# Kernel tuning notes

Measured on AMD Instinct MI355X. Metric: run time of the kernel, lower is better.

Reference implementation:

```python
import jax, jax.numpy as jnp
import numpy as np

N_NODES = 100000


def gcn_conv(x, edge_index, W, b):
    """PyG GCNConv: h = x W^T; add self-loops; symmetric deg^-1/2 norm; scatter-add; + bias."""
    n = x.shape[0]
    src = jnp.concatenate([edge_index[0], jnp.arange(n)])  # self-loops appended
    dst = jnp.concatenate([edge_index[1], jnp.arange(n)])
    deg = jax.ops.segment_sum(jnp.ones_like(dst, dtype=x.dtype), dst, num_segments=n)
    dinv = jnp.where(deg > 0, jax.lax.rsqrt(deg), 0.0)
    norm = dinv[src] * dinv[dst]                             # [E+n]
    h = x @ W.T                                              # [n, out]
    msg = norm[:, None] * h[src]                             # [E+n, out] gather
    out = jax.ops.segment_sum(msg, dst, num_segments=n)      # scatter-add
    return out + b


def setup_inputs() -> dict:
    key = jax.random.key(0)
    ks = jax.random.split(key, 10)
    input_dim, gnn_hidden, tree_hidden, num_classes = 128, 64, 32, 8
    n_edges = 3200000
    x = jax.random.normal(ks[0], (N_NODES, input_dim), dtype=jnp.float32)
    edge_index = jax.random.randint(ks[1], (2, n_edges), 0, N_NODES, dtype=jnp.int64)
    # GCNConv params (PyG Linear weight is [out, in], glorot-ish scale)
    W1 = jax.random.normal(ks[2], (gnn_hidden, input_dim), dtype=jnp.float32) / np.sqrt(input_dim)
    b1 = jnp.zeros((gnn_hidden,), dtype=jnp.float32)
    W2 = jax.random.normal(ks[3], (tree_hidden, gnn_hidden), dtype=jnp.float32) / np.sqrt(gnn_hidden)
    b2 = jnp.zeros((tree_hidden,), dtype=jnp.float32)
    # SoftDecisionTree params (torch.randn init in source)
    gate_w = jax.random.normal(ks[4], (tree_hidden, tree_hidden), dtype=jnp.float32)
    gate_b = jnp.zeros((tree_hidden,), dtype=jnp.float32)
    leaf_w = jax.random.normal(ks[5], (tree_hidden, num_classes), dtype=jnp.float32)
    return {"x": x, "edge_index": edge_index, "W1": W1, "b1": b1, "W2": W2,
            "b2": b2, "gate_w": gate_w, "gate_b": gate_b, "leaf_w": leaf_w}


def reference(x, edge_index, W1, b1, W2, b2, gate_w, gate_b, leaf_w):
    h = jax.nn.relu(gcn_conv(x, edge_index, W1, b1))
    h = gcn_conv(h, edge_index, W2, b2)
    gates = jax.nn.sigmoid(h @ gate_w.T + gate_b)
    return gates @ leaf_w
```

## Files before the change

### kernel.cpp

```cpp
#include <hip/hip_runtime.h>
#include <math.h>

#define IN_DIM 128
#define H1 64
#define H2 32
#define NC 8
#define SCAN_CH 1024
#define NB_MAX 512

typedef unsigned int u32;

__device__ __forceinline__ float bf_lo(u32 u) { return __uint_as_float(u << 16); }
__device__ __forceinline__ float bf_hi(u32 u) { return __uint_as_float(u & 0xffff0000u); }
__device__ __forceinline__ unsigned short f2b(float f) {
  u32 u = __float_as_uint(f);
  u += 0x7fffu + ((u >> 16) & 1u);
  return (unsigned short)(u >> 16);
}


__global__ __launch_bounds__(256) void k_hist(const int* __restrict__ dst,
                                              int* __restrict__ bh,
                                              int E, int EPB, int NBk, int BLK) {
  __shared__ int h[NB_MAX];
  int k = blockIdx.x, tid = threadIdx.x;
  for (int i = tid; i < NBk; i += 256) h[i] = 0;
  __syncthreads();
  int st = k * EPB, en = min(E, st + EPB);
  for (int i = st + tid; i < en; i += 256)
    atomicAdd(&h[((u32)dst[i]) >> 8], 1);
  __syncthreads();
  for (int b = tid; b < NBk; b += 256) bh[b * BLK + k] = h[b];
}


__global__ __launch_bounds__(256) void k_gsc1(const int* __restrict__ A,
                                              int* __restrict__ bsum, int L) {
  int b = blockIdx.x, tid = threadIdx.x;
  int i0 = b * SCAN_CH + tid * 4;
  int s = 0;
  if (i0 + 3 < L) {
    int4 v = *(const int4*)(A + i0);
    s = v.x + v.y + v.z + v.w;
  } else {
    for (int i = i0; i < L; ++i) s += A[i];
  }
  __shared__ int red[256];
  red[tid] = s;
  __syncthreads();
  for (int d = 128; d > 0; d >>= 1) {
    if (tid < d) red[tid] += red[tid + d];
    __syncthreads();
  }
  if (tid == 0) bsum[b] = red[0];
}

__global__ __launch_bounds__(256) void k_gsc2(const int* __restrict__ bsum,
                                              int* __restrict__ bbase,
                                              int* __restrict__ S, int nbk, int L) {
  __shared__ int part[256];
  int tid = threadIdx.x;
  int chunk = (nbk + 255) / 256;
  int st = tid * chunk, en = min(st + chunk, nbk);
  int s = 0;
  for (int i = st; i < en; ++i) s += bsum[i];
  part[tid] = s;
  __syncthreads();
  for (int d = 1; d < 256; d <<= 1) {
    int t = (tid >= d) ? part[tid - d] : 0;
    __syncthreads();
    part[tid] += t;
    __syncthreads();
  }
  int base = (tid == 0) ? 0 : part[tid - 1];
  for (int i = st; i < en; ++i) { bbase[i] = base; base += bsum[i]; }
  if (tid == 255) S[L] = part[255];
}

__global__ __launch_bounds__(256) void k_gsc3(const int* __restrict__ A,
                                              const int* __restrict__ bbase,
                                              int* __restrict__ S, int L) {
  int b = blockIdx.x, tid = threadIdx.x;
  int i0 = b * SCAN_CH + tid * 4;
  int e0 = 0, e1 = 0, e2 = 0, e3 = 0;
  if (i0 + 3 < L) {
    int4 v = *(const int4*)(A + i0);
    e0 = v.x; e1 = v.y; e2 = v.z; e3 = v.w;
  } else {
    if (i0 + 0 < L) e0 = A[i0 + 0];
    if (i0 + 1 < L) e1 = A[i0 + 1];
    if (i0 + 2 < L) e2 = A[i0 + 2];
    if (i0 + 3 < L) e3 = A[i0 + 3];
  }
  __shared__ int part[256];
  part[tid] = e0 + e1 + e2 + e3;
  __syncthreads();
  for (int d = 1; d < 256; d <<= 1) {
    int t = (tid >= d) ? part[tid - d] : 0;
    __syncthreads();
    part[tid] += t;
    __syncthreads();
  }
  int base = bbase[b] + ((tid == 0) ? 0 : part[tid - 1]);
  int o0 = base, o1 = o0 + e0, o2 = o1 + e1, o3 = o2 + e2;
  if (i0 + 3 < L) {
    int4 o; o.x = o0; o.y = o1; o.z = o2; o.w = o3;
    *(int4*)(S + i0) = o;
  } else {
    if (i0 + 0 < L) S[i0 + 0] = o0;
    if (i0 + 1 < L) S[i0 + 1] = o1;
    if (i0 + 2 < L) S[i0 + 2] = o2;
    if (i0 + 3 < L) S[i0 + 3] = o3;
  }
}


__global__ __launch_bounds__(256) void k_scatter(const int* __restrict__ src,
                                                 const int* __restrict__ dst,
                                                 const int* __restrict__ S,
                                                 u32* __restrict__ packed,
                                                 int E, int EPB, int NBk, int BLK) {
  __shared__ int cur[NB_MAX];
  int k = blockIdx.x, tid = threadIdx.x;
  for (int b = tid; b < NBk; b += 256) cur[b] = S[b * BLK + k];
  __syncthreads();
  int st = k * EPB, en = min(E, st + EPB);
  for (int i = st + tid; i < en; i += 256) {
    int d = dst[i];
    int b = ((u32)d) >> 8;
    int pos = atomicAdd(&cur[b], 1);
    packed[pos] = (((u32)d & 255u) << 17) | (u32)src[i];
  }
}


__global__ __launch_bounds__(256) void k_build(const u32* __restrict__ packed,
                                               const int* __restrict__ S,
                                               int* __restrict__ csr,
                                               int* __restrict__ off,
                                               float* __restrict__ dinv,
                                               int n, int NBk, int BLK) {
  __shared__ int cnt[256];
  __shared__ int tmp[256];
  __shared__ int curh[256];
  int b = blockIdx.x, tid = threadIdx.x;
  int r0 = S[b * BLK];
  int r1 = S[(b + 1) * BLK];
  cnt[tid] = 0;
  __syncthreads();
  for (int i = r0 + tid; i < r1; i += 256)
    atomicAdd(&cnt[packed[i] >> 17], 1);
  __syncthreads();
  int v = cnt[tid];
  tmp[tid] = v;
  __syncthreads();
  for (int d = 1; d < 256; d <<= 1) {
    int t = (tid >= d) ? tmp[tid - d] : 0;
    __syncthreads();
    tmp[tid] += t;
    __syncthreads();
  }
  int base = r0 + tmp[tid] - v;
  int node = b * 256 + tid;
  if (node < n) {
    off[node] = base;
    dinv[node] = rsqrtf((float)(v + 1));
  }
  if (b == NBk - 1 && tid == 0) off[n] = r1;
  curh[tid] = base;
  __syncthreads();
  for (int i = r0 + tid; i < r1; i += 256) {
    u32 u = packed[i];
    int pos = atomicAdd(&curh[u >> 17], 1);
    csr[pos] = (int)(u & 0x1FFFFu);
  }
}


__global__ void k_proj1(const float4* __restrict__ x4, const float* __restrict__ W1,
                        const float* __restrict__ dinv,
                        unsigned short* __restrict__ h1p, int n) {
  __shared__ float xs[16][IN_DIM];
  __shared__ float wt[IN_DIM][H1 + 1];
  int tid = threadIdx.x;
  int row0 = blockIdx.x * 16;

  for (int i = tid; i < (H1 * IN_DIM / 4); i += 256) {
    float4 w = ((const float4*)W1)[i];
    int o = (i * 4) / IN_DIM;
    int k = (i * 4) % IN_DIM;
    wt[k + 0][o] = w.x; wt[k + 1][o] = w.y; wt[k + 2][o] = w.z; wt[k + 3][o] = w.w;
  }
  for (int i = tid; i < 16 * IN_DIM / 4; i += 256) {
    int r = (i * 4) / IN_DIM, k = (i * 4) % IN_DIM;
    int row = row0 + r;
    if (row < n)
      *((float4*)&xs[r][k]) = x4[(size_t)row * (IN_DIM / 4) + k / 4];
  }
  __syncthreads();

  int o = tid & 63, rq = tid >> 6;
  float a0 = 0.f, a1 = 0.f, a2 = 0.f, a3 = 0.f;
  for (int k = 0; k < IN_DIM; ++k) {
    float w = wt[k][o];
    a0 += xs[rq * 4 + 0][k] * w;
    a1 += xs[rq * 4 + 1][k] * w;
    a2 += xs[rq * 4 + 2][k] * w;
    a3 += xs[rq * 4 + 3][k] * w;
  }
  int r = row0 + rq * 4;
  if (r + 0 < n) h1p[(size_t)(r + 0) * H1 + o] = f2b(a0 * dinv[r + 0]);
  if (r + 1 < n) h1p[(size_t)(r + 1) * H1 + o] = f2b(a1 * dinv[r + 1]);
  if (r + 2 < n) h1p[(size_t)(r + 2) * H1 + o] = f2b(a2 * dinv[r + 2]);
  if (r + 3 < n) h1p[(size_t)(r + 3) * H1 + o] = f2b(a3 * dinv[r + 3]);
}


__global__ __launch_bounds__(256) void k_agg64_proj2(
    const u32* __restrict__ hp,
    const float* __restrict__ dinv,
    const int* __restrict__ off, const int* __restrict__ csr,
    const float* __restrict__ b1, const float* __restrict__ W2,
    unsigned short* __restrict__ h2p, int n) {
  __shared__ float wt[H1][H2 + 1];
  __shared__ float rows[4][H1];
  int tid = threadIdx.x;

  for (int i = tid; i < H2 * H1 / 4; i += 256) {
    float4 w = ((const float4*)W2)[i];
    int o = (i * 4) / H1, k = (i * 4) % H1;
    wt[k + 0][o] = w.x; wt[k + 1][o] = w.y; wt[k + 2][o] = w.z; wt[k + 3][o] = w.w;
  }

  int lane = tid & 63;
  int wv = __builtin_amdgcn_readfirstlane(tid >> 6);
  int wid0 = blockIdx.x * 4 + wv;
  int wid = wid0 < n ? wid0 : n - 1;
  int half = lane >> 5, f2 = lane & 31;

  float ax = 0.f, ay = 0.f;
  if (half == 0) {
    u32 u = hp[(size_t)wid * (H1 / 2) + f2];
    ax = bf_lo(u); ay = bf_hi(u);
  }
  int r0 = off[wid], r1 = off[wid + 1];
  int i = r0 + half;
  for (; i + 6 < r1; i += 8) {
    int s0 = csr[i + 0], s1 = csr[i + 2], s2 = csr[i + 4], s3 = csr[i + 6];
    u32 u0 = hp[(size_t)s0 * (H1 / 2) + f2];
    u32 u1 = hp[(size_t)s1 * (H1 / 2) + f2];
    u32 u2 = hp[(size_t)s2 * (H1 / 2) + f2];
    u32 u3 = hp[(size_t)s3 * (H1 / 2) + f2];
    ax += bf_lo(u0); ay += bf_hi(u0);
    ax += bf_lo(u1); ay += bf_hi(u1);
    ax += bf_lo(u2); ay += bf_hi(u2);
    ax += bf_lo(u3); ay += bf_hi(u3);
  }
  for (; i < r1; i += 2) {
    u32 u = hp[(size_t)csr[i] * (H1 / 2) + f2];
    ax += bf_lo(u);
    ay += bf_hi(u);
  }
  ax += __shfl_down(ax, 32, 64);
  ay += __shfl_down(ay, 32, 64);
  float d = dinv[wid];
  if (half == 0) {
    float2 rv;
    rv.x = fmaxf(ax * d + b1[2 * f2 + 0], 0.f);
    rv.y = fmaxf(ay * d + b1[2 * f2 + 1], 0.f);
    *(float2*)&rows[wv][2 * f2] = rv;
  }
  __syncthreads();

  int o = lane & 31;
  float a = 0.f;
#pragma unroll
  for (int k = 0; k < 32; ++k) {
    int kk = half * 32 + k;
    a += rows[wv][kk] * wt[kk][o];
  }
  a += __shfl_down(a, 32, 64);
  if (half == 0 && wid0 < n) h2p[(size_t)wid0 * H2 + o] = f2b(a * d);
}


__global__ __launch_bounds__(256) void k_agg32_tree(
    const u32* __restrict__ hp,
    const float* __restrict__ dinv,
    const int* __restrict__ off, const int* __restrict__ csr,
    const float* __restrict__ b2, const float* __restrict__ gate_w,
    const float* __restrict__ gate_b, const float* __restrict__ leaf_w,
    float* __restrict__ out, int n) {
  __shared__ float gwt[H2][H2 + 1];
  __shared__ float lws[H2][NC + 1];
  __shared__ float rowh[4][H2];
  __shared__ float rowg[4][H2];
  int tid = threadIdx.x;

  {
    float4 w = ((const float4*)gate_w)[tid];
    int j = (tid * 4) / H2, k = (tid * 4) % H2;
    gwt[k + 0][j] = w.x; gwt[k + 1][j] = w.y; gwt[k + 2][j] = w.z; gwt[k + 3][j] = w.w;
  }
  lws[tid >> 3][tid & 7] = leaf_w[tid];

  int lane = tid & 63;
  int wv = __builtin_amdgcn_readfirstlane(tid >> 6);
  int wid0 = blockIdx.x * 4 + wv;
  int wid = wid0 < n ? wid0 : n - 1;
  int q = lane >> 4, f2 = lane & 15;

  float ax = 0.f, ay = 0.f;
  if (q == 0) {
    u32 u = hp[(size_t)wid * (H2 / 2) + f2];
    ax = bf_lo(u); ay = bf_hi(u);
  }
  int r0 = off[wid], r1 = off[wid + 1];
  int i = r0 + q;
  for (; i + 12 < r1; i += 16) {
    int s0 = csr[i + 0], s1 = csr[i + 4], s2 = csr[i + 8], s3 = csr[i + 12];
    u32 u0 = hp[(size_t)s0 * (H2 / 2) + f2];
    u32 u1 = hp[(size_t)s1 * (H2 / 2) + f2];
    u32 u2 = hp[(size_t)s2 * (H2 / 2) + f2];
    u32 u3 = hp[(size_t)s3 * (H2 / 2) + f2];
    ax += bf_lo(u0); ay += bf_hi(u0);
    ax += bf_lo(u1); ay += bf_hi(u1);
    ax += bf_lo(u2); ay += bf_hi(u2);
    ax += bf_lo(u3); ay += bf_hi(u3);
  }
  for (; i < r1; i += 4) {
    u32 u = hp[(size_t)csr[i] * (H2 / 2) + f2];
    ax += bf_lo(u);
    ay += bf_hi(u);
  }
  ax += __shfl_down(ax, 32, 64); ay += __shfl_down(ay, 32, 64);
  ax += __shfl_down(ax, 16, 64); ay += __shfl_down(ay, 16, 64);
  float d = dinv[wid];
  if (lane < 16) {
    float2 rv;
    rv.x = ax * d + b2[2 * f2 + 0];
    rv.y = ay * d + b2[2 * f2 + 1];
    *(float2*)&rowh[wv][2 * f2] = rv;
  }
  __syncthreads();

  int half = lane >> 5, f = lane & 31;
  float g = 0.f;
#pragma unroll
  for (int k = 0; k < 16; ++k) {
    int kk = half * 16 + k;
    g += rowh[wv][kk] * gwt[kk][f];
  }
  g += __shfl_down(g, 32, 64);
  if (half == 0) rowg[wv][f] = 1.0f / (1.0f + __expf(-(g + gate_b[f])));
  __syncthreads();

  int c = lane & 7, gi = lane >> 3;
  float a = 0.f;
#pragma unroll
  for (int j4 = 0; j4 < 4; ++j4) {
    int jj = gi * 4 + j4;
    a += rowg[wv][jj] * lws[jj][c];
  }
  a += __shfl_down(a, 32, 64);
  a += __shfl_down(a, 16, 64);
  a += __shfl_down(a, 8, 64);
  if (lane < 8 && wid0 < n) out[(size_t)wid0 * NC + lane] = a;
}


extern "C" void kernel_launch(void* const* d_in, const int* in_sizes, int n_in,
                              void* d_out, int out_size, void* d_ws, size_t ws_size,
                              hipStream_t stream) {
  const float* x  = (const float*)d_in[0];
  const int*   ei = (const int*)d_in[1];
  const float* W1 = (const float*)d_in[2];
  const float* b1 = (const float*)d_in[3];
  const float* W2 = (const float*)d_in[4];
  const float* b2 = (const float*)d_in[5];
  const float* gw = (const float*)d_in[6];
  const float* gb = (const float*)d_in[7];
  const float* lw = (const float*)d_in[8];
  float* out = (float*)d_out;

  int n = in_sizes[0] / IN_DIM;
  int E = in_sizes[1] / 2;
  const int* src  = ei;
  const int* dstp = ei + E;

  int NBk = (n + 255) >> 8;
  int BLK = 512;
  int EPB = (E + BLK - 1) / BLK;
  int L   = NBk * BLK;
  int nbs = (L + SCAN_CH - 1) / SCAN_CH;

  size_t n4  = ((size_t)n + 3) & ~(size_t)3;
  size_t np4 = ((size_t)n + 1 + 3) & ~(size_t)3;
  size_t E4  = ((size_t)E + 3) & ~(size_t)3;
  size_t L4  = ((size_t)L + 1 + 3) & ~(size_t)3;
  size_t nbs4 = ((size_t)nbs + 3) & ~(size_t)3;
  char* w = (char*)d_ws;
  int* csr    = (int*)w;   w += E4 * 4;
  u32* packed = (u32*)w;   w += E4 * 4;
  int* bh     = (int*)w;   w += L4 * 4;
  int* S      = (int*)w;   w += L4 * 4;
  int* bsum   = (int*)w;   w += nbs4 * 4;
  int* bbase  = (int*)w;   w += nbs4 * 4;
  float* dinv = (float*)w; w += n4 * 4;
  int* off    = (int*)w;   w += np4 * 4;
  unsigned short* h1p = (unsigned short*)w;  w += n4 * (size_t)H1 * 2;
  unsigned short* h2p = (unsigned short*)w;

  int gw4 = (n + 3) / 4;

  k_hist<<<BLK, 256, 0, stream>>>(dstp, bh, E, EPB, NBk, BLK);
  k_gsc1<<<nbs, 256, 0, stream>>>(bh, bsum, L);
  k_gsc2<<<1, 256, 0, stream>>>(bsum, bbase, S, nbs, L);
  k_gsc3<<<nbs, 256, 0, stream>>>(bh, bbase, S, L);
  k_scatter<<<BLK, 256, 0, stream>>>(src, dstp, S, packed, E, EPB, NBk, BLK);
  k_build<<<NBk, 256, 0, stream>>>(packed, S, csr, off, dinv, n, NBk, BLK);

  k_proj1<<<(n + 15) / 16, 256, 0, stream>>>((const float4*)x, W1, dinv, h1p, n);
  k_agg64_proj2<<<gw4, 256, 0, stream>>>((const u32*)h1p, dinv, off, csr, b1, W2, h2p, n);
  k_agg32_tree<<<gw4, 256, 0, stream>>>((const u32*)h2p, dinv, off, csr, b2, gw, gb, lw, out, n);
}
```

Before: 411.0 us.

## Sort CSR neighbors by source group and deepen gather unroll in layer-1 aggregation

The CSR build kernel now keeps a per-destination sub-histogram over 32 coarse source-id groups in shared memory, so each node's neighbor list comes out roughly sorted by source index. This should improve locality of the later feature gathers. The layer-1 aggregation loop is unrolled from 4 to 8 independent gathers per iteration to keep more loads in flight. BLK also becomes a compile-time constant. In exchange, the build kernel uses about 33 KB more shared memory, which may lower its occupancy, and adds a serial 32-step per-thread scan.

Result: slower. 429.1 us (+4.4%).

```diff
diff --git a/kernel.cpp b/kernel.cpp
--- a/kernel.cpp
+++ b/kernel.cpp
@@ -7,6 +7,7 @@
 #define NC 8
 #define SCAN_CH 1024
 #define NB_MAX 512
+#define BLK 512
 
 typedef unsigned int u32;
 
@@ -21,7 +22,7 @@
 
 __global__ __launch_bounds__(256) void k_hist(const int* __restrict__ dst,
                                               int* __restrict__ bh,
-                                              int E, int EPB, int NBk, int BLK) {
+                                              int E, int EPB, int NBk) {
   __shared__ int h[NB_MAX];
   int k = blockIdx.x, tid = threadIdx.x;
   for (int i = tid; i < NBk; i += 256) h[i] = 0;
@@ -119,7 +120,7 @@
                                                  const int* __restrict__ dst,
                                                  const int* __restrict__ S,
                                                  u32* __restrict__ packed,
-                                                 int E, int EPB, int NBk, int BLK) {
+                                                 int E, int EPB, int NBk) {
   __shared__ int cur[NB_MAX];
   int k = blockIdx.x, tid = threadIdx.x;
   for (int b = tid; b < NBk; b += 256) cur[b] = S[b * BLK + k];
@@ -139,20 +140,30 @@
                                                int* __restrict__ csr,
                                                int* __restrict__ off,
                                                float* __restrict__ dinv,
-                                               int n, int NBk, int BLK) {
+                                               int n, int NBk) {
+  __shared__ int h2[256 * 33];
   __shared__ int cnt[256];
   __shared__ int tmp[256];
-  __shared__ int curh[256];
   int b = blockIdx.x, tid = threadIdx.x;
   int r0 = S[b * BLK];
   int r1 = S[(b + 1) * BLK];
-  cnt[tid] = 0;
-  __syncthreads();
-  for (int i = r0 + tid; i < r1; i += 256)
-    atomicAdd(&cnt[packed[i] >> 17], 1);
-  __syncthreads();
-  int v = cnt[tid];
-  tmp[tid] = v;
+  for (int i = tid; i < 256 * 33; i += 256) h2[i] = 0;
+  __syncthreads();
+  for (int i = r0 + tid; i < r1; i += 256) {
+    u32 u = packed[i];
+    atomicAdd(&h2[(u >> 17) * 33 + ((u & 0x1FFFFu) >> 12)], 1);
+  }
+  __syncthreads();
+  {
+    int d = 0;
+    for (int g = 0; g < 32; ++g) {
+      int t = h2[tid * 33 + g];
+      h2[tid * 33 + g] = d;
+      d += t;
+    }
+    cnt[tid] = d;
+    tmp[tid] = d;
+  }
   __syncthreads();
   for (int d = 1; d < 256; d <<= 1) {
     int t = (tid >= d) ? tmp[tid - d] : 0;
@@ -160,18 +171,20 @@
     tmp[tid] += t;
     __syncthreads();
   }
-  int base = r0 + tmp[tid] - v;
+  int base = r0 + tmp[tid] - cnt[tid];
   int node = b * 256 + tid;
   if (node < n) {
     off[node] = base;
-    dinv[node] = rsqrtf((float)(v + 1));
+    dinv[node] = rsqrtf((float)(cnt[tid] + 1));
   }
   if (b == NBk - 1 && tid == 0) off[n] = r1;
-  curh[tid] = base;
+  {
+    for (int g = 0; g < 32; ++g) h2[tid * 33 + g] += base;
+  }
   __syncthreads();
   for (int i = r0 + tid; i < r1; i += 256) {
     u32 u = packed[i];
-    int pos = atomicAdd(&curh[u >> 17], 1);
+    int pos = atomicAdd(&h2[(u >> 17) * 33 + ((u & 0x1FFFFu) >> 12)], 1);
     csr[pos] = (int)(u & 0x1FFFFu);
   }
 }
@@ -245,16 +258,25 @@
   }
   int r0 = off[wid], r1 = off[wid + 1];
   int i = r0 + half;
-  for (; i + 6 < r1; i += 8) {
-    int s0 = csr[i + 0], s1 = csr[i + 2], s2 = csr[i + 4], s3 = csr[i + 6];
+  for (; i + 14 < r1; i += 16) {
+    int s0 = csr[i + 0],  s1 = csr[i + 2],  s2 = csr[i + 4],  s3 = csr[i + 6];
+    int s4 = csr[i + 8],  s5 = csr[i + 10], s6 = csr[i + 12], s7 = csr[i + 14];
     u32 u0 = hp[(size_t)s0 * (H1 / 2) + f2];
     u32 u1 = hp[(size_t)s1 * (H1 / 2) + f2];
     u32 u2 = hp[(size_t)s2 * (H1 / 2) + f2];
     u32 u3 = hp[(size_t)s3 * (H1 / 2) + f2];
+    u32 u4 = hp[(size_t)s4 * (H1 / 2) + f2];
+    u32 u5 = hp[(size_t)s5 * (H1 / 2) + f2];
+    u32 u6 = hp[(size_t)s6 * (H1 / 2) + f2];
+    u32 u7 = hp[(size_t)s7 * (H1 / 2) + f2];
     ax += bf_lo(u0); ay += bf_hi(u0);
     ax += bf_lo(u1); ay += bf_hi(u1);
     ax += bf_lo(u2); ay += bf_hi(u2);
     ax += bf_lo(u3); ay += bf_hi(u3);
+    ax += bf_lo(u4); ay += bf_hi(u4);
+    ax += bf_lo(u5); ay += bf_hi(u5);
+    ax += bf_lo(u6); ay += bf_hi(u6);
+    ax += bf_lo(u7); ay += bf_hi(u7);
   }
   for (; i < r1; i += 2) {
     u32 u = hp[(size_t)csr[i] * (H1 / 2) + f2];
@@ -389,7 +411,6 @@
   const int* dstp = ei + E;
 
   int NBk = (n + 255) >> 8;
-  int BLK = 512;
   int EPB = (E + BLK - 1) / BLK;
   int L   = NBk * BLK;
   int nbs = (L + SCAN_CH - 1) / SCAN_CH;
@@ -413,12 +434,12 @@
 
   int gw4 = (n + 3) / 4;
 
-  k_hist<<<BLK, 256, 0, stream>>>(dstp, bh, E, EPB, NBk, BLK);
+  k_hist<<<BLK, 256, 0, stream>>>(dstp, bh, E, EPB, NBk);
   k_gsc1<<<nbs, 256, 0, stream>>>(bh, bsum, L);
   k_gsc2<<<1, 256, 0, stream>>>(bsum, bbase, S, nbs, L);
   k_gsc3<<<nbs, 256, 0, stream>>>(bh, bbase, S, L);
-  k_scatter<<<BLK, 256, 0, stream>>>(src, dstp, S, packed, E, EPB, NBk, BLK);
-  k_build<<<NBk, 256, 0, stream>>>(packed, S, csr, off, dinv, n, NBk, BLK);
+  k_scatter<<<BLK, 256, 0, stream>>>(src, dstp, S, packed, E, EPB, NBk);
+  k_build<<<NBk, 256, 0, stream>>>(packed, S, csr, off, dinv, n, NBk);
 
   k_proj1<<<(n + 15) / 16, 256, 0, stream>>>((const float4*)x, W1, dinv, h1p, n);
   k_agg64_proj2<<<gw4, 256, 0, stream>>>((const u32*)h1p, dinv, off, csr, b1, W2, h2p, n);
```
